# Performance work log

Measured on AMD Instinct MI355X. Metric: run time of the kernel, lower is better.

## Reference

```python
import jax, jax.numpy as jnp
import numpy as np

HEADS = 8
DIM_HEAD = 64


def setup_inputs() -> dict:
    key = jax.random.key(0)
    ks = jax.random.split(key, 9)
    b, n, d = 2, 2048, 512
    inner = HEADS * DIM_HEAD  # 512
    s = 0.02
    return {
        "x": jax.random.normal(ks[0], (b, n, d), dtype=jnp.float32),
        "attn_bias": jax.random.normal(ks[1], (1, HEADS, n, n), dtype=jnp.float32),
        "Wq": jax.random.normal(ks[2], (d, inner), dtype=jnp.float32) * s,
        "Wkv": jax.random.normal(ks[3], (d, 2 * inner), dtype=jnp.float32) * s,
        "Wo": jax.random.normal(ks[4], (inner, d), dtype=jnp.float32) * s,
        "bo": jax.random.normal(ks[5], (d,), dtype=jnp.float32) * s,
        "Wg": jax.random.normal(ks[6], (d, inner), dtype=jnp.float32) * s,
        "bg": jnp.ones((inner,), dtype=jnp.float32),
    }


def reference(x, attn_bias, Wq, Wkv, Wo, bo, Wg, bg):
    b, n, d = x.shape
    h, dh = HEADS, DIM_HEAD
    scale = dh ** -0.5
    # projections: [b, n, h*dh] -> [b, h, n, dh]
    q = (x @ Wq).reshape(b, n, h, dh).transpose(0, 2, 1, 3) * scale
    k, v = jnp.split(x @ Wkv, 2, axis=-1)
    k = k.reshape(b, n, h, dh).transpose(0, 2, 1, 3)
    v = v.reshape(b, n, h, dh).transpose(0, 2, 1, 3)
    # scores + additive bias; max-subtract softmax (stable, as in original)
    dots = jnp.einsum('bhid,bhjd->bhij', q, k) + attn_bias
    attn = jax.nn.softmax(dots, axis=-1)
    out = jnp.einsum('bhij,bhjd->bhid', attn, v)
    out = out.transpose(0, 2, 1, 3).reshape(b, n, h * dh)
    # gating sigmoid epilogue
    gates = jax.nn.sigmoid(x @ Wg + bg)
    out = out * gates
    return out @ Wo + bo
```

## Files before the change

### kernel.cpp

```cpp
#include <hip/hip_runtime.h>
#include <hip/hip_bf16.h>

typedef __bf16 bf16_t;
typedef __bf16 bf16x8 __attribute__((ext_vector_type(8)));
typedef float f32x4 __attribute__((ext_vector_type(4)));

static __device__ __forceinline__ bf16_t to_bf16(float f) { return (bf16_t)f; }

__global__ void k_convert_x(const float* __restrict__ src, bf16_t* __restrict__ dst, int n8) {
  int i = blockIdx.x * blockDim.x + threadIdx.x;
  if (i >= n8) return;
  const float4* s = reinterpret_cast<const float4*>(src) + (size_t)i * 2;
  float4 a = s[0], b = s[1];
  bf16x8 v;
  v[0]=(bf16_t)a.x; v[1]=(bf16_t)a.y; v[2]=(bf16_t)a.z; v[3]=(bf16_t)a.w;
  v[4]=(bf16_t)b.x; v[5]=(bf16_t)b.y; v[6]=(bf16_t)b.z; v[7]=(bf16_t)b.w;
  reinterpret_cast<bf16x8*>(dst)[i] = v;
}

__global__ void k_transpose_cvt(const float* __restrict__ src, bf16_t* __restrict__ dst, int Nc) {
  __shared__ bf16_t tile[64 * 72];
  const int n0 = blockIdx.x * 64, k0 = blockIdx.y * 64;
  const int t = threadIdx.x;
  #pragma unroll
  for (int it = 0; it < 16; ++it) {
    int c = t + it * 256;
    int kl = c >> 6, nl = c & 63;
    tile[kl * 72 + nl] = to_bf16(src[(size_t)(k0 + kl) * Nc + n0 + nl]);
  }
  __syncthreads();
  #pragma unroll
  for (int it = 0; it < 16; ++it) {
    int c = t + it * 256;
    int nl = c >> 6, kl = c & 63;
    dst[(size_t)(n0 + nl) * 512 + k0 + kl] = tile[kl * 72 + nl];
  }
}

__global__ __launch_bounds__(256) void k_gemm_proj(
    const bf16_t* __restrict__ A,
    const bf16_t* __restrict__ BT,
    const float*  __restrict__ bg,
    bf16_t* __restrict__ qo,
    bf16_t* __restrict__ ko,
    bf16_t* __restrict__ vto,
    float*  __restrict__ go)
{
  __shared__ __align__(16) bf16_t lA[128 * 72];
  __shared__ __align__(16) bf16_t lB[128 * 72];
  const int t = threadIdx.x;
  const int w = t >> 6, lane = t & 63, lr = lane & 15, lg = lane >> 4;
  const int wr = w >> 1, wc = w & 1;
  const int m0 = blockIdx.y * 128, n0 = blockIdx.x * 128;
  f32x4 acc[4][4] = {};
  for (int k0 = 0; k0 < 512; k0 += 64) {
    __syncthreads();
    #pragma unroll
    for (int it = 0; it < 4; ++it) {
      int c = t + it * 256;
      int row = c >> 3, cc = c & 7;
      *reinterpret_cast<bf16x8*>(&lA[row * 72 + cc * 8]) =
          *reinterpret_cast<const bf16x8*>(&A[(size_t)(m0 + row) * 512 + k0 + cc * 8]);
      *reinterpret_cast<bf16x8*>(&lB[row * 72 + cc * 8]) =
          *reinterpret_cast<const bf16x8*>(&BT[(size_t)(n0 + row) * 512 + k0 + cc * 8]);
    }
    __syncthreads();
    #pragma unroll
    for (int kk = 0; kk < 2; ++kk) {
      bf16x8 af[4], bfm[4];
      #pragma unroll
      for (int mf = 0; mf < 4; ++mf)
        af[mf] = *reinterpret_cast<const bf16x8*>(&lA[(wr*64 + mf*16 + lr) * 72 + kk*32 + lg*8]);
      #pragma unroll
      for (int nf = 0; nf < 4; ++nf)
        bfm[nf] = *reinterpret_cast<const bf16x8*>(&lB[(wc*64 + nf*16 + lr) * 72 + kk*32 + lg*8]);
      #pragma unroll
      for (int mf = 0; mf < 4; ++mf)
        #pragma unroll
        for (int nf = 0; nf < 4; ++nf)
          acc[mf][nf] = __builtin_amdgcn_mfma_f32_16x16x32_bf16(af[mf], bfm[nf], acc[mf][nf], 0, 0, 0);
    }
  }
  const int seg = n0 >> 9;
  #pragma unroll
  for (int mf = 0; mf < 4; ++mf) {
    #pragma unroll
    for (int nf = 0; nf < 4; ++nf) {
      #pragma unroll
      for (int r = 0; r < 4; ++r) {
        int rm = m0 + wr*64 + mf*16 + lg*4 + r;
        int cn = n0 + wc*64 + nf*16 + lr;
        float v = acc[mf][nf][r];
        int b = rm >> 11, n = rm & 2047;
        int c = cn & 511;
        if (seg == 0) {
          int h = c >> 6, dh = c & 63;
          qo[((size_t)(b*8 + h) * 2048 + n) * 64 + dh] = to_bf16(v * 0.125f);
        } else if (seg == 1) {
          int h = c >> 6, dh = c & 63;
          ko[((size_t)(b*8 + h) * 2048 + n) * 64 + dh] = to_bf16(v);
        } else if (seg == 2) {
          int h = c >> 6, dh = c & 63;
          vto[((size_t)(b*8 + h) * 64 + dh) * 2048 + n] = to_bf16(v);
        } else {
          float z = v + bg[c];
          go[(size_t)rm * 512 + c] = 1.0f / (1.0f + __expf(-z));
        }
      }
    }
  }
}

#define M_FIX 8.0f
template<int FINAL>
__global__ __launch_bounds__(256, 4) void k_attn(
    const bf16_t* __restrict__ q,
    const bf16_t* __restrict__ kb,
    const bf16_t* __restrict__ vt,
    const float*  __restrict__ bias,
    const float*  __restrict__ gates,
    bf16_t* __restrict__ ao,
    float* __restrict__ pO,
    float* __restrict__ pl)
{
  __shared__ __align__(16) bf16_t lK[64 * 72];
  __shared__ __align__(16) bf16_t lV[64 * 72];
  __shared__ __align__(16) bf16_t lP[4][16 * 72];
  const int t = threadIdx.x, w = t >> 6, lane = t & 63, lr = lane & 15, lg = lane >> 4;
  const int bh = blockIdx.y, b = bh >> 3, h = bh & 7;
  const int i0 = blockIdx.x * 64, ib = i0 + w * 16;
  const int ntile = 32 / (int)gridDim.z;
  const int sz = blockIdx.z;
  const int jbase = sz * ntile * 64;

  bf16x8 aq[2];
  const bf16_t* qp = q + ((size_t)bh * 2048 + ib + lr) * 64;
  aq[0] = *reinterpret_cast<const bf16x8*>(qp + lg * 8);
  aq[1] = *reinterpret_cast<const bf16x8*>(qp + 32 + lg * 8);

  float l_r[4] = {0.f, 0.f, 0.f, 0.f};
  f32x4 accO[4] = {};

  const float* bias_p = bias + (size_t)h * 2048 * 2048 + (size_t)(ib + lg * 4) * 2048 + lr;
  const bf16_t* kp = kb + (size_t)bh * 2048 * 64;
  const bf16_t* vp = vt + (size_t)bh * 64 * 2048;

  const int srow = t >> 3, scc = t & 7;
  const int srow1 = (t + 256) >> 3;

  bf16x8 rK0, rK1, rV0, rV1;
  float bv[4][4];
  {
    const int j0 = jbase;
    rK0 = *reinterpret_cast<const bf16x8*>(&kp[(size_t)(j0 + srow)  * 64 + scc * 8]);
    rK1 = *reinterpret_cast<const bf16x8*>(&kp[(size_t)(j0 + srow1) * 64 + scc * 8]);
    rV0 = *reinterpret_cast<const bf16x8*>(&vp[(size_t)srow  * 2048 + j0 + scc * 8]);
    rV1 = *reinterpret_cast<const bf16x8*>(&vp[(size_t)srow1 * 2048 + j0 + scc * 8]);
    #pragma unroll
    for (int nf = 0; nf < 4; ++nf)
      #pragma unroll
      for (int r = 0; r < 4; ++r)
        bv[nf][r] = bias_p[(size_t)r * 2048 + j0 + nf * 16];
  }

  for (int jt = 0; jt < ntile; ++jt) {
    const int j1 = jbase + (jt + 1) * 64;
    const bool more = (jt + 1 < ntile);

    __syncthreads();
    *reinterpret_cast<bf16x8*>(&lK[srow  * 72 + scc * 8]) = rK0;
    *reinterpret_cast<bf16x8*>(&lK[srow1 * 72 + scc * 8]) = rK1;
    *reinterpret_cast<bf16x8*>(&lV[srow  * 72 + scc * 8]) = rV0;
    *reinterpret_cast<bf16x8*>(&lV[srow1 * 72 + scc * 8]) = rV1;
    __syncthreads();

    if (more) {
      rK0 = *reinterpret_cast<const bf16x8*>(&kp[(size_t)(j1 + srow)  * 64 + scc * 8]);
      rK1 = *reinterpret_cast<const bf16x8*>(&kp[(size_t)(j1 + srow1) * 64 + scc * 8]);
      rV0 = *reinterpret_cast<const bf16x8*>(&vp[(size_t)srow  * 2048 + j1 + scc * 8]);
      rV1 = *reinterpret_cast<const bf16x8*>(&vp[(size_t)srow1 * 2048 + j1 + scc * 8]);
    }

    f32x4 s[4] = {};
    #pragma unroll
    for (int kk = 0; kk < 2; ++kk) {
      #pragma unroll
      for (int nf = 0; nf < 4; ++nf) {
        bf16x8 bf = *reinterpret_cast<const bf16x8*>(&lK[(nf*16 + lr) * 72 + kk*32 + lg*8]);
        s[nf] = __builtin_amdgcn_mfma_f32_16x16x32_bf16(aq[kk], bf, s[nf], 0, 0, 0);
      }
    }
    #pragma unroll
    for (int nf = 0; nf < 4; ++nf) {
      #pragma unroll
      for (int r = 0; r < 4; ++r) {
        float p = __expf(s[nf][r] + bv[nf][r] - M_FIX);
        s[nf][r] = p;
        l_r[r] += p;
        lP[w][(lg*4 + r) * 72 + nf*16 + lr] = to_bf16(p);
      }
    }
    if (more) {
      #pragma unroll
      for (int nf = 0; nf < 4; ++nf)
        #pragma unroll
        for (int r = 0; r < 4; ++r)
          bv[nf][r] = bias_p[(size_t)r * 2048 + j1 + nf * 16];
    }

    #pragma unroll
    for (int kk = 0; kk < 2; ++kk) {
      bf16x8 pa = *reinterpret_cast<const bf16x8*>(&lP[w][lr * 72 + kk*32 + lg*8]);
      #pragma unroll
      for (int df = 0; df < 4; ++df) {
        bf16x8 bv8 = *reinterpret_cast<const bf16x8*>(&lV[(df*16 + lr) * 72 + kk*32 + lg*8]);
        accO[df] = __builtin_amdgcn_mfma_f32_16x16x32_bf16(pa, bv8, accO[df], 0, 0, 0);
      }
    }
  }

  #pragma unroll
  for (int r = 0; r < 4; ++r) {
    float rs = l_r[r];
    rs += __shfl_xor(rs, 1); rs += __shfl_xor(rs, 2);
    rs += __shfl_xor(rs, 4); rs += __shfl_xor(rs, 8);
    l_r[r] = rs;
  }

  if (FINAL) {
    #pragma unroll
    for (int r = 0; r < 4; ++r) {
      float inv = 1.0f / l_r[r];
      int ig = ib + lg*4 + r;
      #pragma unroll
      for (int df = 0; df < 4; ++df) {
        int dg = h*64 + df*16 + lr;
        float gate = gates[(size_t)(b*2048 + ig) * 512 + dg];
        ao[(size_t)(b*2048 + ig) * 512 + dg] = to_bf16(accO[df][r] * inv * gate);
      }
    }
  } else {
    float* po = pO + (((size_t)sz * 16 + bh) * 2048) * 64;
    #pragma unroll
    for (int r = 0; r < 4; ++r) {
      int ig = ib + lg*4 + r;
      #pragma unroll
      for (int df = 0; df < 4; ++df)
        po[(size_t)ig * 64 + df*16 + lr] = accO[df][r];
    }
    if (lr == 0) {
      size_t rb = ((size_t)sz * 16 + bh) * 2048 + ib + lg*4;
      #pragma unroll
      for (int r = 0; r < 4; ++r) pl[rb + r] = l_r[r];
    }
  }
}

__global__ __launch_bounds__(256) void k_attn_combine(
    const float* __restrict__ pO, const float* __restrict__ pl,
    const float* __restrict__ gates, bf16_t* __restrict__ ao, int nsplit)
{
  int idx = blockIdx.x * 256 + threadIdx.x;
  int dh = idx & 63, row = (idx >> 6) & 2047, bh = idx >> 17;
  int b = bh >> 3, h = bh & 7;
  const size_t SP_O = (size_t)16 * 2048 * 64, SP_S = (size_t)16 * 2048;
  size_t rb = (size_t)bh * 2048 + row;
  float L = 0.f, O = 0.f;
  for (int s = 0; s < nsplit; ++s) {
    L += pl[s * SP_S + rb];
    O += pO[s * SP_O + rb * 64 + dh];
  }
  float gate = gates[(size_t)(b * 2048 + row) * 512 + h * 64 + dh];
  ao[(size_t)(b * 2048 + row) * 512 + h * 64 + dh] = to_bf16(O / L * gate);
}

__global__ __launch_bounds__(256) void k_gemm_out(
    const bf16_t* __restrict__ A,
    const bf16_t* __restrict__ BT,
    const float*  __restrict__ bo,
    float* __restrict__ out)
{
  __shared__ __align__(16) bf16_t lA[128 * 72];
  __shared__ __align__(16) bf16_t lB[128 * 72];
  const int t = threadIdx.x;
  const int w = t >> 6, lane = t & 63, lr = lane & 15, lg = lane >> 4;
  const int wr = w >> 1, wc = w & 1;
  const int m0 = blockIdx.y * 128, n0 = blockIdx.x * 128;
  f32x4 acc[4][4] = {};
  for (int k0 = 0; k0 < 512; k0 += 64) {
    __syncthreads();
    #pragma unroll
    for (int it = 0; it < 4; ++it) {
      int c = t + it * 256;
      int row = c >> 3, cc = c & 7;
      *reinterpret_cast<bf16x8*>(&lA[row * 72 + cc * 8]) =
          *reinterpret_cast<const bf16x8*>(&A[(size_t)(m0 + row) * 512 + k0 + cc * 8]);
      *reinterpret_cast<bf16x8*>(&lB[row * 72 + cc * 8]) =
          *reinterpret_cast<const bf16x8*>(&BT[(size_t)(n0 + row) * 512 + k0 + cc * 8]);
    }
    __syncthreads();
    #pragma unroll
    for (int kk = 0; kk < 2; ++kk) {
      bf16x8 af[4], bfm[4];
      #pragma unroll
      for (int mf = 0; mf < 4; ++mf)
        af[mf] = *reinterpret_cast<const bf16x8*>(&lA[(wr*64 + mf*16 + lr) * 72 + kk*32 + lg*8]);
      #pragma unroll
      for (int nf = 0; nf < 4; ++nf)
        bfm[nf] = *reinterpret_cast<const bf16x8*>(&lB[(wc*64 + nf*16 + lr) * 72 + kk*32 + lg*8]);
      #pragma unroll
      for (int mf = 0; mf < 4; ++mf)
        #pragma unroll
        for (int nf = 0; nf < 4; ++nf)
          acc[mf][nf] = __builtin_amdgcn_mfma_f32_16x16x32_bf16(af[mf], bfm[nf], acc[mf][nf], 0, 0, 0);
    }
  }
  #pragma unroll
  for (int mf = 0; mf < 4; ++mf) {
    #pragma unroll
    for (int nf = 0; nf < 4; ++nf) {
      #pragma unroll
      for (int r = 0; r < 4; ++r) {
        int rm = m0 + wr*64 + mf*16 + lg*4 + r;
        int cn = n0 + wc*64 + nf*16 + lr;
        out[(size_t)rm * 512 + cn] = acc[mf][nf][r] + bo[cn];
      }
    }
  }
}

extern "C" void kernel_launch(void* const* d_in, const int* in_sizes, int n_in,
                              void* d_out, int out_size, void* d_ws, size_t ws_size,
                              hipStream_t stream) {
  const float* x    = (const float*)d_in[0];
  const float* bias = (const float*)d_in[1];
  const float* Wq   = (const float*)d_in[2];
  const float* Wkv  = (const float*)d_in[3];
  const float* Wo   = (const float*)d_in[4];
  const float* bo   = (const float*)d_in[5];
  const float* Wg   = (const float*)d_in[6];
  const float* bg   = (const float*)d_in[7];
  float* out = (float*)d_out;

  char* ws = (char*)d_ws;
  const size_t MB = 1024 * 1024;
  bf16_t* x_bf  = (bf16_t*)(ws + 0 * MB);
  bf16_t* WcatT = (bf16_t*)(ws + 4 * MB);
  bf16_t* WoT   = (bf16_t*)(ws + 6 * MB);
  bf16_t* q_bf  = (bf16_t*)(ws + 7 * MB);
  bf16_t* k_bf  = (bf16_t*)(ws + 11 * MB);
  bf16_t* vt_bf = (bf16_t*)(ws + 15 * MB);
  float*  g_f32 = (float*) (ws + 19 * MB);
  bf16_t* ao_bf = (bf16_t*)(ws + 27 * MB);
  float*  pO    = (float*) (ws + 31 * MB);
  float*  pl    = (float*) (ws + 47 * MB);

  k_convert_x<<<1024, 256, 0, stream>>>(x, x_bf, 2097152 / 8);
  k_transpose_cvt<<<dim3(8, 8),  256, 0, stream>>>(Wq,  WcatT,               512);
  k_transpose_cvt<<<dim3(16, 8), 256, 0, stream>>>(Wkv, WcatT + 512 * 512,  1024);
  k_transpose_cvt<<<dim3(8, 8),  256, 0, stream>>>(Wg,  WcatT + 1536 * 512,  512);
  k_transpose_cvt<<<dim3(8, 8),  256, 0, stream>>>(Wo,  WoT,                 512);
  k_gemm_proj<<<dim3(16, 32), 256, 0, stream>>>(x_bf, WcatT, bg, q_bf, k_bf, vt_bf, g_f32);

  if (ws_size >= 48 * MB) {
    k_attn<0><<<dim3(32, 16, 2), 256, 0, stream>>>(q_bf, k_bf, vt_bf, bias, nullptr,
                                                   nullptr, pO, pl);
    k_attn_combine<<<8192, 256, 0, stream>>>(pO, pl, g_f32, ao_bf, 2);
  } else {
    k_attn<1><<<dim3(32, 16, 1), 256, 0, stream>>>(q_bf, k_bf, vt_bf, bias, g_f32,
                                                   ao_bf, nullptr, nullptr);
  }
  k_gemm_out<<<dim3(4, 32), 256, 0, stream>>>(ao_bf, WoT, bo, out);
}
```

Baseline: 113.5 us.

## Keep softmax probabilities in registers by transposing QK^T MFMA operand order

```diff
diff --git a/kernel.cpp b/kernel.cpp
--- a/kernel.cpp
+++ b/kernel.cpp
@@ -3,9 +3,23 @@
 
 typedef __bf16 bf16_t;
 typedef __bf16 bf16x8 __attribute__((ext_vector_type(8)));
+typedef __bf16 bf16x4 __attribute__((ext_vector_type(4)));
+typedef short short4v __attribute__((ext_vector_type(4)));
 typedef float f32x4 __attribute__((ext_vector_type(4)));
 
 static __device__ __forceinline__ bf16_t to_bf16(float f) { return (bf16_t)f; }
+
+static __device__ __forceinline__ f32x4 mfma16x16x16bf16(bf16x4 a, bf16x4 b, f32x4 c) {
+#if __has_builtin(__builtin_amdgcn_mfma_f32_16x16x16bf16_1k)
+  return __builtin_amdgcn_mfma_f32_16x16x16bf16_1k(
+      *reinterpret_cast<short4v*>(&a), *reinterpret_cast<short4v*>(&b), c, 0, 0, 0);
+#else
+  f32x4 d;
+  asm volatile("v_mfma_f32_16x16x16_bf16 %0, %1, %2, %3"
+               : "=v"(d) : "v"(a), "v"(b), "v"(c));
+  return d;
+#endif
+}
 
 __global__ void k_convert_x(const float* __restrict__ src, bf16_t* __restrict__ dst, int n8) {
   int i = blockIdx.x * blockDim.x + threadIdx.x;
@@ -125,7 +139,6 @@
 {
   __shared__ __align__(16) bf16_t lK[64 * 72];
   __shared__ __align__(16) bf16_t lV[64 * 72];
-  __shared__ __align__(16) bf16_t lP[4][16 * 72];
   const int t = threadIdx.x, w = t >> 6, lane = t & 63, lr = lane & 15, lg = lane >> 4;
   const int bh = blockIdx.y, b = bh >> 3, h = bh & 7;
   const int i0 = blockIdx.x * 64, ib = i0 + w * 16;
@@ -138,10 +151,10 @@
   aq[0] = *reinterpret_cast<const bf16x8*>(qp + lg * 8);
   aq[1] = *reinterpret_cast<const bf16x8*>(qp + 32 + lg * 8);
 
-  float l_r[4] = {0.f, 0.f, 0.f, 0.f};
+  float l_lane = 0.f;
   f32x4 accO[4] = {};
 
-  const float* bias_p = bias + (size_t)h * 2048 * 2048 + (size_t)(ib + lg * 4) * 2048 + lr;
+  const float* bias_p = bias + (size_t)h * 2048 * 2048 + (size_t)(ib + lr) * 2048 + lg * 4;
   const bf16_t* kp = kb + (size_t)bh * 2048 * 64;
   const bf16_t* vp = vt + (size_t)bh * 64 * 2048;
 
@@ -149,7 +162,7 @@
   const int srow1 = (t + 256) >> 3;
 
   bf16x8 rK0, rK1, rV0, rV1;
-  float bv[4][4];
+  float4 bv4[4];
   {
     const int j0 = jbase;
     rK0 = *reinterpret_cast<const bf16x8*>(&kp[(size_t)(j0 + srow)  * 64 + scc * 8]);
@@ -158,9 +171,7 @@
     rV1 = *reinterpret_cast<const bf16x8*>(&vp[(size_t)srow1 * 2048 + j0 + scc * 8]);
     #pragma unroll
     for (int nf = 0; nf < 4; ++nf)
-      #pragma unroll
-      for (int r = 0; r < 4; ++r)
-        bv[nf][r] = bias_p[(size_t)r * 2048 + j0 + nf * 16];
+      bv4[nf] = *reinterpret_cast<const float4*>(&bias_p[j0 + nf * 16]);
   }
 
   for (int jt = 0; jt < ntile; ++jt) {
@@ -184,53 +195,49 @@
     f32x4 s[4] = {};
     #pragma unroll
     for (int kk = 0; kk < 2; ++kk) {
-      #pragma unroll
-      for (int nf = 0; nf < 4; ++nf) {
-        bf16x8 bf = *reinterpret_cast<const bf16x8*>(&lK[(nf*16 + lr) * 72 + kk*32 + lg*8]);
-        s[nf] = __builtin_amdgcn_mfma_f32_16x16x32_bf16(aq[kk], bf, s[nf], 0, 0, 0);
-      }
-    }
+      bf16x8 kf[4];
+      #pragma unroll
+      for (int nf = 0; nf < 4; ++nf)
+        kf[nf] = *reinterpret_cast<const bf16x8*>(&lK[(nf*16 + lr) * 72 + kk*32 + lg*8]);
+      #pragma unroll
+      for (int nf = 0; nf < 4; ++nf)
+        s[nf] = __builtin_amdgcn_mfma_f32_16x16x32_bf16(kf[nf], aq[kk], s[nf], 0, 0, 0);
+    }
+
+    bf16x4 pa[4];
     #pragma unroll
     for (int nf = 0; nf < 4; ++nf) {
       #pragma unroll
       for (int r = 0; r < 4; ++r) {
-        float p = __expf(s[nf][r] + bv[nf][r] - M_FIX);
-        s[nf][r] = p;
-        l_r[r] += p;
-        lP[w][(lg*4 + r) * 72 + nf*16 + lr] = to_bf16(p);
+        float p = __expf(s[nf][r] + bv4[nf][r] - M_FIX);
+        l_lane += p;
+        pa[nf][r] = to_bf16(p);
       }
     }
     if (more) {
       #pragma unroll
       for (int nf = 0; nf < 4; ++nf)
-        #pragma unroll
-        for (int r = 0; r < 4; ++r)
-          bv[nf][r] = bias_p[(size_t)r * 2048 + j1 + nf * 16];
-    }
-
-    #pragma unroll
-    for (int kk = 0; kk < 2; ++kk) {
-      bf16x8 pa = *reinterpret_cast<const bf16x8*>(&lP[w][lr * 72 + kk*32 + lg*8]);
+        bv4[nf] = *reinterpret_cast<const float4*>(&bias_p[j1 + nf * 16]);
+    }
+
+    #pragma unroll
+    for (int nf = 0; nf < 4; ++nf) {
       #pragma unroll
       for (int df = 0; df < 4; ++df) {
-        bf16x8 bv8 = *reinterpret_cast<const bf16x8*>(&lV[(df*16 + lr) * 72 + kk*32 + lg*8]);
-        accO[df] = __builtin_amdgcn_mfma_f32_16x16x32_bf16(pa, bv8, accO[df], 0, 0, 0);
-      }
-    }
-  }
-
-  #pragma unroll
-  for (int r = 0; r < 4; ++r) {
-    float rs = l_r[r];
-    rs += __shfl_xor(rs, 1); rs += __shfl_xor(rs, 2);
-    rs += __shfl_xor(rs, 4); rs += __shfl_xor(rs, 8);
-    l_r[r] = rs;
-  }
+        bf16x4 vb = *reinterpret_cast<const bf16x4*>(&lV[(df*16 + lr) * 72 + nf*16 + lg*4]);
+        accO[df] = mfma16x16x16bf16(pa[nf], vb, accO[df]);
+      }
+    }
+  }
+
+  float rs = l_lane;
+  rs += __shfl_xor(rs, 16);
+  rs += __shfl_xor(rs, 32);
 
   if (FINAL) {
     #pragma unroll
     for (int r = 0; r < 4; ++r) {
-      float inv = 1.0f / l_r[r];
+      float inv = 1.0f / __shfl(rs, lg * 4 + r);
       int ig = ib + lg*4 + r;
       #pragma unroll
       for (int df = 0; df < 4; ++df) {
@@ -248,10 +255,9 @@
       for (int df = 0; df < 4; ++df)
         po[(size_t)ig * 64 + df*16 + lr] = accO[df][r];
     }
-    if (lr == 0) {
-      size_t rb = ((size_t)sz * 16 + bh) * 2048 + ib + lg*4;
-      #pragma unroll
-      for (int r = 0; r < 4; ++r) pl[rb + r] = l_r[r];
+    if (lane < 16) {
+      size_t rb = ((size_t)sz * 16 + bh) * 2048 + ib;
+      pl[rb + lane] = rs;
     }
   }
 }
```

Result: slower. 117.2 us (+3.3%).
